# Optimization experiments

Hardware: AMD Instinct MI355X
Metric: run time of the kernel (lower is better)

## Reference

```python
import jax, jax.numpy as jnp
import numpy as np

P_DROP = 0.25
DROP_KEY_SEED = 42  # fixed seed makes dropout deterministic for baseline comparison


def setup_inputs() -> dict:
    key = jax.random.key(0)
    k1, k2, k3, k4 = jax.random.split(key, 4)
    B, S, D, DV = 16, 2048, 64, 512
    x1 = jax.random.normal(k1, (B, S, D), dtype=jnp.float32)   # queries [B,S,64]
    m = jax.random.normal(k2, (D, DV), dtype=jnp.float32)      # [64,512]
    n = jax.random.normal(k3, (S, DV), dtype=jnp.float32)      # [S,512]
    q = jax.random.normal(k4, (S, DV), dtype=jnp.float32)      # values [S,512]
    return {"x1": x1, "m": m, "n": n, "q": q}


def reference(x1, m, n, q):
    scale = jnp.float32(1.0 / 64.0)  # hard-coded in original (not 1/sqrt(d))
    kT = jnp.matmul(m, n.T)                        # matmul5: [64, S]
    scores = jnp.matmul(x1, kT) * scale            # [B, S, S]
    probs = jax.nn.softmax(scores, axis=-1)        # softmax over last dim
    keep = jax.random.bernoulli(jax.random.key(DROP_KEY_SEED), 1.0 - P_DROP, probs.shape)
    probs = jnp.where(keep, probs / (1.0 - P_DROP), jnp.float32(0.0))  # dropout (train mode)
    return jnp.matmul(probs, q)                    # [B, S, DV]
```

## Files before the change

### kernel.cpp

```cpp
#include <hip/hip_runtime.h>


typedef short  s8v __attribute__((ext_vector_type(8)));
typedef float  f4v __attribute__((ext_vector_type(4)));

__device__ __forceinline__ unsigned short f2bf(float f) {
  unsigned int u = __float_as_uint(f);
  u += 0x7fffu + ((u >> 16) & 1u);
  return (unsigned short)(u >> 16);
}
__device__ __forceinline__ float bf2f(unsigned short h) {
  return __uint_as_float(((unsigned int)h) << 16);
}
__device__ __forceinline__ unsigned int pack_bf2(float a, float b) {
  unsigned int ua = __float_as_uint(a);
  ua += 0x7fffu + ((ua >> 16) & 1u);
  unsigned int ub = __float_as_uint(b);
  ub += 0x7fffu + ((ub >> 16) & 1u);
  return (ua >> 16) | (ub & 0xffff0000u);
}

__device__ __forceinline__ unsigned int rotl(unsigned int x, unsigned int r) {
  return __builtin_amdgcn_alignbit(x, x, 32u - r);
}

__device__ __forceinline__ unsigned int jax_bits(unsigned int idx) {
  const unsigned int K0 = 0u, K1 = 42u, K2 = 0x1BD11BDAu ^ K0 ^ K1;
  unsigned int x0 = 0u, x1 = idx;
  x0 += K0; x1 += K1;
#define TF_R(r) { x0 += x1; x1 = rotl(x1, r); x1 ^= x0; }
  TF_R(13) TF_R(15) TF_R(26) TF_R(6)
  x0 += K1; x1 += K2 + 1u;
  TF_R(17) TF_R(29) TF_R(16) TF_R(24)
  x0 += K2; x1 += K0 + 2u;
  TF_R(13) TF_R(15) TF_R(26) TF_R(6)
  x0 += K0; x1 += K1 + 3u;
  TF_R(17) TF_R(29) TF_R(16) TF_R(24)
  x0 += K1; x1 += K2 + 4u;
  TF_R(13) TF_R(15) TF_R(26) TF_R(6)
  x0 += K2; x1 += K0 + 5u;
#undef TF_R
  return x0 ^ x1;
}

__device__ __forceinline__ f4v mfma16(s8v a, s8v b, f4v c) {
  return __builtin_amdgcn_mfma_f32_16x16x32_bf16(a, b, c, 0, 0, 0);
}

__global__ void prep_misc(const float* __restrict__ x1, const float* __restrict__ q,
                          const float* __restrict__ m,
                          unsigned short* __restrict__ Xhi,
                          unsigned short* __restrict__ qT,
                          float* __restrict__ mT) {
  const int blk = blockIdx.x;
  const int t = threadIdx.x;
  if (blk < 1024) {
    const int i = (blk * 256 + t) * 8;
    float4 a = *(const float4*)&x1[i];
    float4 b = *(const float4*)&x1[i + 4];
    ushort4 o0, o1;
    o0.x = f2bf(a.x); o0.y = f2bf(a.y); o0.z = f2bf(a.z); o0.w = f2bf(a.w);
    o1.x = f2bf(b.x); o1.y = f2bf(b.y); o1.z = f2bf(b.z); o1.w = f2bf(b.w);
    *(ushort4*)&Xhi[i] = o0;
    *(ushort4*)&Xhi[i + 4] = o1;
  } else if (blk < 1280) {
    __shared__ unsigned short tile[64][65];
    const int bb = blk - 1024;
    const int s0 = (bb >> 3) * 64;
    const int d0 = (bb & 7) * 64;
#pragma unroll
    for (int k = 0; k < 16; ++k) {
      int lin = t + k * 256;
      int r = lin >> 6, c = lin & 63;
      tile[c][r] = f2bf(q[(size_t)(s0 + r) * 512 + d0 + c]);
    }
    __syncthreads();
#pragma unroll
    for (int k = 0; k < 16; ++k) {
      int lin = t + k * 256;
      int rr = lin >> 6, cc = lin & 63;
      qT[(size_t)(d0 + rr) * 2048 + s0 + cc] = tile[rr][cc];
    }
  } else {
    const int i = (blk - 1280) * 256 + t;
    int dv = i >> 6, d = i & 63;
    mT[i] = m[d * 512 + dv];
  }
}

__global__ void build_k(const float* __restrict__ mT, const float* __restrict__ n,
                        unsigned short* __restrict__ Khi, unsigned short* __restrict__ Klo) {
  const int s = blockIdx.x * 4 + (threadIdx.x >> 6);
  const int d = threadIdx.x & 63;
  const float* nrow = n + (size_t)s * 512;
  float a0 = 0.f, a1 = 0.f, a2 = 0.f, a3 = 0.f;
  for (int dv = 0; dv < 512; dv += 4) {
    a0 = fmaf(mT[(dv + 0) * 64 + d], nrow[dv + 0], a0);
    a1 = fmaf(mT[(dv + 1) * 64 + d], nrow[dv + 1], a1);
    a2 = fmaf(mT[(dv + 2) * 64 + d], nrow[dv + 2], a2);
    a3 = fmaf(mT[(dv + 3) * 64 + d], nrow[dv + 3], a3);
  }
  float k = ((a0 + a1) + (a2 + a3)) * 0.015625f;
  unsigned short h = f2bf(k);
  Khi[s * 64 + d] = h;
  Klo[s * 64 + d] = f2bf(k - bf2f(h));
}

__global__ __launch_bounds__(512, 4) void attn_main(
    const unsigned short* __restrict__ Xhi,
    const unsigned short* __restrict__ Khi, const unsigned short* __restrict__ Klo,
    const unsigned short* __restrict__ qT, float* __restrict__ out) {
  __shared__ unsigned short Ks[2][128][72];
  __shared__ unsigned short Ps[64][136];
  __shared__ float rsum[2][64];

  const int tid  = threadIdx.x;
  const int wave = tid >> 6;
  const int lane = tid & 63;
  const int l15  = lane & 15;
  const int quad = lane >> 4;

  const int b    = blockIdx.x >> 5;
  const int row0 = (blockIdx.x & 31) * 64;

  const int qk_row = (wave & 3) * 16 + l15;
  const int qk_kg  = (wave >> 2) * 64;

  const size_t xg = ((size_t)(b * 2048 + row0 + qk_row)) * 64 + quad * 8;
  const s8v X0 = *(const s8v*)&Xhi[xg];
  const s8v X1 = *(const s8v*)&Xhi[xg + 32];

  f4v acc[4][4];
#pragma unroll
  for (int mt = 0; mt < 4; ++mt)
#pragma unroll
    for (int nt = 0; nt < 4; ++nt) acc[mt][nt] = f4v{0.f, 0.f, 0.f, 0.f};
  float rs = 0.f;

  const unsigned int idx_row =
      ((unsigned int)(b * 2048 + row0 + qk_row)) * 2048u;

  for (int it = 0; it < 16; ++it) {
    const int kt = it * 128;
    __syncthreads();
    {
      const int kk = tid >> 2, c = (tid & 3) * 16;
      const size_t g = ((size_t)(kt + kk)) * 64 + c;
      *(uint4*)&Ks[0][kk][c]     = *(const uint4*)&Khi[g];
      *(uint4*)&Ks[0][kk][c + 8] = *(const uint4*)&Khi[g + 8];
      *(uint4*)&Ks[1][kk][c]     = *(const uint4*)&Klo[g];
      *(uint4*)&Ks[1][kk][c + 8] = *(const uint4*)&Klo[g + 8];
    }
    __syncthreads();

#pragma unroll
    for (int nt = 0; nt < 4; ++nt) {
      const int key = qk_kg + nt * 16 + l15;
      s8v Kh0 = *(const s8v*)&Ks[0][key][quad * 8];
      s8v Kh1 = *(const s8v*)&Ks[0][key][32 + quad * 8];
      s8v Kl0 = *(const s8v*)&Ks[1][key][quad * 8];
      s8v Kl1 = *(const s8v*)&Ks[1][key][32 + quad * 8];
      f4v c = {0.f, 0.f, 0.f, 0.f};
      c = mfma16(Kh0, X0, c);  c = mfma16(Kh1, X1, c);
      c = mfma16(Kl0, X0, c);  c = mfma16(Kl1, X1, c);
      const unsigned int idx0 = idx_row + (unsigned int)(kt + qk_kg + nt * 16 + quad * 4);
      float p[4];
#pragma unroll
      for (int r = 0; r < 4; ++r) {
        float e = __expf(c[r]);
        rs += e;
        const unsigned int bits = jax_bits(idx0 + r);
        p[r] = (bits < 0xC0000000u) ? e : 0.0f;
      }
      const unsigned int p01 = pack_bf2(p[0], p[1]);
      const unsigned int p23 = pack_bf2(p[2], p[3]);
      *(uint2*)&Ps[(wave & 3) * 16 + l15][qk_kg + nt * 16 + quad * 4] =
          make_uint2(p01, p23);
    }
    __syncthreads();

#pragma unroll
    for (int ks = 0; ks < 4; ++ks) {
      s8v Va[4];
#pragma unroll
      for (int mt = 0; mt < 4; ++mt) {
        const size_t g =
            (size_t)(wave * 64 + mt * 16 + l15) * 2048 + kt + ks * 32 + quad * 8;
        Va[mt] = *(const s8v*)&qT[g];
      }
#pragma unroll
      for (int nt = 0; nt < 4; ++nt) {
        s8v Pb = *(const s8v*)&Ps[nt * 16 + l15][ks * 32 + quad * 8];
#pragma unroll
        for (int mt = 0; mt < 4; ++mt) acc[mt][nt] = mfma16(Va[mt], Pb, acc[mt][nt]);
      }
    }
  }

  {
    float v = rs;
    v += __shfl_xor(v, 16);
    v += __shfl_xor(v, 32);
    if (quad == 0) rsum[wave >> 2][(wave & 3) * 16 + l15] = v;
  }
  __syncthreads();

#pragma unroll
  for (int nt = 0; nt < 4; ++nt) {
    const int rloc = nt * 16 + l15;
    const int row = row0 + rloc;
    const float inv = 1.0f / (0.75f * (rsum[0][rloc] + rsum[1][rloc]));
    const size_t base = ((size_t)(b * 2048 + row)) * 512 + wave * 64;
#pragma unroll
    for (int mt = 0; mt < 4; ++mt) {
      f4v v = acc[mt][nt];
      v[0] *= inv; v[1] *= inv; v[2] *= inv; v[3] *= inv;
      *(f4v*)&out[base + mt * 16 + quad * 4] = v;
    }
  }
}

extern "C" void kernel_launch(void* const* d_in, const int* in_sizes, int n_in,
                              void* d_out, int out_size, void* d_ws, size_t ws_size,
                              hipStream_t stream) {
  (void)in_sizes; (void)n_in; (void)out_size; (void)ws_size;
  const float* x1 = (const float*)d_in[0];
  const float* m  = (const float*)d_in[1];
  const float* n  = (const float*)d_in[2];
  const float* q  = (const float*)d_in[3];
  float* out = (float*)d_out;

  char* ws = (char*)d_ws;
  float*          mT  = (float*)(ws + 0);
  unsigned short* Khi = (unsigned short*)(ws + 131072);
  unsigned short* Klo = (unsigned short*)(ws + 393216);
  unsigned short* Xhi = (unsigned short*)(ws + 655360);
  unsigned short* qT  = (unsigned short*)(ws + 4849664);

  prep_misc<<<1408, 256, 0, stream>>>(x1, q, m, Xhi, qT, mT);
  build_k<<<512, 256, 0, stream>>>(mT, n, Khi, Klo);
  attn_main<<<512, 512, 0, stream>>>(Xhi, Khi, Klo, qT, out);
}
```

Baseline: 321.7 us.

## Merge prep kernels, read K straight from global, double-buffer P, use exp2

Folds the m transpose and the K build into one prep kernel that stages m chunks in shared memory, which removes a launch and the mT round trip. The attention kernel stops staging K in LDS and reads K fragments directly from global/L2. P is double-buffered, which drops two barriers per iteration. It also folds log2(e) into K so exp2 can be used, switches to a hardware packed bf16 convert, and raises wave priority around the PV MFMAs. Direct global K loads may add latency that the LDS staging used to hide.

Result: slower. 353.7 us (+9.9%).

```diff
diff --git a/kernel.cpp b/kernel.cpp
--- a/kernel.cpp
+++ b/kernel.cpp
@@ -11,13 +11,6 @@
 }
 __device__ __forceinline__ float bf2f(unsigned short h) {
   return __uint_as_float(((unsigned int)h) << 16);
-}
-__device__ __forceinline__ unsigned int pack_bf2(float a, float b) {
-  unsigned int ua = __float_as_uint(a);
-  ua += 0x7fffu + ((ua >> 16) & 1u);
-  unsigned int ub = __float_as_uint(b);
-  ub += 0x7fffu + ((ub >> 16) & 1u);
-  return (ua >> 16) | (ub & 0xffff0000u);
 }
 
 __device__ __forceinline__ unsigned int rotl(unsigned int x, unsigned int r) {
@@ -47,15 +40,43 @@
   return __builtin_amdgcn_mfma_f32_16x16x32_bf16(a, b, c, 0, 0, 0);
 }
 
-__global__ void prep_misc(const float* __restrict__ x1, const float* __restrict__ q,
-                          const float* __restrict__ m,
-                          unsigned short* __restrict__ Xhi,
-                          unsigned short* __restrict__ qT,
-                          float* __restrict__ mT) {
+__global__ void prep_all(const float* __restrict__ x1, const float* __restrict__ q,
+                         const float* __restrict__ m, const float* __restrict__ nmat,
+                         unsigned short* __restrict__ Xhi, unsigned short* __restrict__ qT,
+                         unsigned short* __restrict__ Khi, unsigned short* __restrict__ Klo) {
   const int blk = blockIdx.x;
   const int t = threadIdx.x;
-  if (blk < 1024) {
-    const int i = (blk * 256 + t) * 8;
+  if (blk < 512) {
+    __shared__ float Lm[64][68];
+    const int s = blk * 4 + (t >> 6);
+    const int d = t & 63;
+    float a0 = 0.f, a1 = 0.f, a2 = 0.f, a3 = 0.f;
+    for (int ch = 0; ch < 8; ++ch) {
+      const int dv0 = ch * 64;
+      __syncthreads();
+#pragma unroll
+      for (int k = 0; k < 4; ++k) {
+        const int fi = t + k * 256;
+        const int row = fi >> 4, c4 = fi & 15;
+        *(float4*)&Lm[row][c4 * 4] =
+            *(const float4*)&m[(size_t)row * 512 + dv0 + c4 * 4];
+      }
+      __syncthreads();
+      const float4* nv = (const float4*)&nmat[(size_t)s * 512 + dv0];
+#pragma unroll
+      for (int j4 = 0; j4 < 16; ++j4) {
+        const float4 nf = nv[j4];
+        const float4 mf = *(const float4*)&Lm[d][j4 * 4];
+        a0 = fmaf(mf.x, nf.x, a0); a1 = fmaf(mf.y, nf.y, a1);
+        a2 = fmaf(mf.z, nf.z, a2); a3 = fmaf(mf.w, nf.w, a3);
+      }
+    }
+    const float kv = ((a0 + a1) + (a2 + a3)) * (1.44269504088896340736f / 64.0f);
+    const unsigned short h = f2bf(kv);
+    Khi[s * 64 + d] = h;
+    Klo[s * 64 + d] = f2bf(kv - bf2f(h));
+  } else if (blk < 1536) {
+    const int i = ((blk - 512) * 256 + t) * 8;
     float4 a = *(const float4*)&x1[i];
     float4 b = *(const float4*)&x1[i + 4];
     ushort4 o0, o1;
@@ -63,9 +84,9 @@
     o1.x = f2bf(b.x); o1.y = f2bf(b.y); o1.z = f2bf(b.z); o1.w = f2bf(b.w);
     *(ushort4*)&Xhi[i] = o0;
     *(ushort4*)&Xhi[i + 4] = o1;
-  } else if (blk < 1280) {
+  } else {
     __shared__ unsigned short tile[64][65];
-    const int bb = blk - 1024;
+    const int bb = blk - 1536;
     const int s0 = (bb >> 3) * 64;
     const int d0 = (bb & 7) * 64;
 #pragma unroll
@@ -81,37 +102,14 @@
       int rr = lin >> 6, cc = lin & 63;
       qT[(size_t)(d0 + rr) * 2048 + s0 + cc] = tile[rr][cc];
     }
-  } else {
-    const int i = (blk - 1280) * 256 + t;
-    int dv = i >> 6, d = i & 63;
-    mT[i] = m[d * 512 + dv];
-  }
-}
-
-__global__ void build_k(const float* __restrict__ mT, const float* __restrict__ n,
-                        unsigned short* __restrict__ Khi, unsigned short* __restrict__ Klo) {
-  const int s = blockIdx.x * 4 + (threadIdx.x >> 6);
-  const int d = threadIdx.x & 63;
-  const float* nrow = n + (size_t)s * 512;
-  float a0 = 0.f, a1 = 0.f, a2 = 0.f, a3 = 0.f;
-  for (int dv = 0; dv < 512; dv += 4) {
-    a0 = fmaf(mT[(dv + 0) * 64 + d], nrow[dv + 0], a0);
-    a1 = fmaf(mT[(dv + 1) * 64 + d], nrow[dv + 1], a1);
-    a2 = fmaf(mT[(dv + 2) * 64 + d], nrow[dv + 2], a2);
-    a3 = fmaf(mT[(dv + 3) * 64 + d], nrow[dv + 3], a3);
-  }
-  float k = ((a0 + a1) + (a2 + a3)) * 0.015625f;
-  unsigned short h = f2bf(k);
-  Khi[s * 64 + d] = h;
-  Klo[s * 64 + d] = f2bf(k - bf2f(h));
+  }
 }
 
 __global__ __launch_bounds__(512, 4) void attn_main(
     const unsigned short* __restrict__ Xhi,
     const unsigned short* __restrict__ Khi, const unsigned short* __restrict__ Klo,
     const unsigned short* __restrict__ qT, float* __restrict__ out) {
-  __shared__ unsigned short Ks[2][128][72];
-  __shared__ unsigned short Ps[64][136];
+  __shared__ unsigned short Ps[2][64][136];
   __shared__ float rsum[2][64];
 
   const int tid  = threadIdx.x;
@@ -140,26 +138,21 @@
   const unsigned int idx_row =
       ((unsigned int)(b * 2048 + row0 + qk_row)) * 2048u;
 
+  const unsigned short* __restrict__ khp = Khi + ((qk_kg + l15) * 64 + quad * 8);
+  const unsigned short* __restrict__ klp = Klo + ((qk_kg + l15) * 64 + quad * 8);
+  const unsigned short* __restrict__ qvp = qT + ((wave * 64 + l15) * 2048 + quad * 8);
+
   for (int it = 0; it < 16; ++it) {
     const int kt = it * 128;
-    __syncthreads();
-    {
-      const int kk = tid >> 2, c = (tid & 3) * 16;
-      const size_t g = ((size_t)(kt + kk)) * 64 + c;
-      *(uint4*)&Ks[0][kk][c]     = *(const uint4*)&Khi[g];
-      *(uint4*)&Ks[0][kk][c + 8] = *(const uint4*)&Khi[g + 8];
-      *(uint4*)&Ks[1][kk][c]     = *(const uint4*)&Klo[g];
-      *(uint4*)&Ks[1][kk][c + 8] = *(const uint4*)&Klo[g + 8];
-    }
-    __syncthreads();
+    unsigned short (*Pb)[136] = Ps[it & 1];
 
 #pragma unroll
     for (int nt = 0; nt < 4; ++nt) {
-      const int key = qk_kg + nt * 16 + l15;
-      s8v Kh0 = *(const s8v*)&Ks[0][key][quad * 8];
-      s8v Kh1 = *(const s8v*)&Ks[0][key][32 + quad * 8];
-      s8v Kl0 = *(const s8v*)&Ks[1][key][quad * 8];
-      s8v Kl1 = *(const s8v*)&Ks[1][key][32 + quad * 8];
+      const int ko = (kt + nt * 16) * 64;
+      s8v Kh0 = *(const s8v*)(khp + ko);
+      s8v Kh1 = *(const s8v*)(khp + ko + 32);
+      s8v Kl0 = *(const s8v*)(klp + ko);
+      s8v Kl1 = *(const s8v*)(klp + ko + 32);
       f4v c = {0.f, 0.f, 0.f, 0.f};
       c = mfma16(Kh0, X0, c);  c = mfma16(Kh1, X1, c);
       c = mfma16(Kl0, X0, c);  c = mfma16(Kl1, X1, c);
@@ -167,14 +160,15 @@
       float p[4];
 #pragma unroll
       for (int r = 0; r < 4; ++r) {
-        float e = __expf(c[r]);
+        float e = exp2f(c[r]);
         rs += e;
         const unsigned int bits = jax_bits(idx0 + r);
         p[r] = (bits < 0xC0000000u) ? e : 0.0f;
       }
-      const unsigned int p01 = pack_bf2(p[0], p[1]);
-      const unsigned int p23 = pack_bf2(p[2], p[3]);
-      *(uint2*)&Ps[(wave & 3) * 16 + l15][qk_kg + nt * 16 + quad * 4] =
+      unsigned int p01, p23;
+      asm("v_cvt_pk_bf16_f32 %0, %1, %2" : "=v"(p01) : "v"(p[0]), "v"(p[1]));
+      asm("v_cvt_pk_bf16_f32 %0, %1, %2" : "=v"(p23) : "v"(p[2]), "v"(p[3]));
+      *(uint2*)&Pb[(wave & 3) * 16 + l15][qk_kg + nt * 16 + quad * 4] =
           make_uint2(p01, p23);
     }
     __syncthreads();
@@ -183,17 +177,16 @@
     for (int ks = 0; ks < 4; ++ks) {
       s8v Va[4];
 #pragma unroll
-      for (int mt = 0; mt < 4; ++mt) {
-        const size_t g =
-            (size_t)(wave * 64 + mt * 16 + l15) * 2048 + kt + ks * 32 + quad * 8;
-        Va[mt] = *(const s8v*)&qT[g];
-      }
+      for (int mt = 0; mt < 4; ++mt)
+        Va[mt] = *(const s8v*)(qvp + mt * (16 * 2048) + kt + ks * 32);
+      __builtin_amdgcn_s_setprio(1);
 #pragma unroll
       for (int nt = 0; nt < 4; ++nt) {
-        s8v Pb = *(const s8v*)&Ps[nt * 16 + l15][ks * 32 + quad * 8];
-#pragma unroll
-        for (int mt = 0; mt < 4; ++mt) acc[mt][nt] = mfma16(Va[mt], Pb, acc[mt][nt]);
-      }
+        s8v Pf = *(const s8v*)&Pb[nt * 16 + l15][ks * 32 + quad * 8];
+#pragma unroll
+        for (int mt = 0; mt < 4; ++mt) acc[mt][nt] = mfma16(Va[mt], Pf, acc[mt][nt]);
+      }
+      __builtin_amdgcn_s_setprio(0);
     }
   }
 
@@ -231,13 +224,11 @@
   float* out = (float*)d_out;
 
   char* ws = (char*)d_ws;
-  float*          mT  = (float*)(ws + 0);
-  unsigned short* Khi = (unsigned short*)(ws + 131072);
-  unsigned short* Klo = (unsigned short*)(ws + 393216);
-  unsigned short* Xhi = (unsigned short*)(ws + 655360);
-  unsigned short* qT  = (unsigned short*)(ws + 4849664);
-
-  prep_misc<<<1408, 256, 0, stream>>>(x1, q, m, Xhi, qT, mT);
-  build_k<<<512, 256, 0, stream>>>(mT, n, Khi, Klo);
+  unsigned short* Khi = (unsigned short*)(ws);
+  unsigned short* Klo = (unsigned short*)(ws + 262144);
+  unsigned short* Xhi = (unsigned short*)(ws + 524288);
+  unsigned short* qT  = (unsigned short*)(ws + 4718592);
+
+  prep_all<<<1792, 256, 0, stream>>>(x1, q, m, n, Xhi, qT, Khi, Klo);
   attn_main<<<512, 512, 0, stream>>>(Xhi, Khi, Klo, qT, out);
 }
```
